# Kernel optimization log

Hardware: AMD Instinct MI355X
Metric: run time of the kernel (lower is better)

## Reference

```python
import jax, jax.numpy as jnp
import numpy as np
import math

INPUT_SIZE = 1024
OUTPUT_SIZE = 1024
QK_SIZE = 1024
B, S = 4, 2048


def setup_inputs() -> dict:
    key = jax.random.key(0)
    ks = jax.random.split(key, 7)
    scale = 1.0 / math.sqrt(INPUT_SIZE)
    return {
        "x": jax.random.normal(ks[0], (B, S, INPUT_SIZE), dtype=jnp.float32),
        "Wq": jax.random.uniform(ks[1], (QK_SIZE, INPUT_SIZE), minval=-scale, maxval=scale, dtype=jnp.float32),
        "bq": jax.random.uniform(ks[2], (QK_SIZE,), minval=-scale, maxval=scale, dtype=jnp.float32),
        "Wk": jax.random.uniform(ks[3], (QK_SIZE, INPUT_SIZE), minval=-scale, maxval=scale, dtype=jnp.float32),
        "bk": jax.random.uniform(ks[4], (QK_SIZE,), minval=-scale, maxval=scale, dtype=jnp.float32),
        "Wv": jax.random.uniform(ks[5], (OUTPUT_SIZE, INPUT_SIZE), minval=-scale, maxval=scale, dtype=jnp.float32),
        "bv": jax.random.uniform(ks[6], (OUTPUT_SIZE,), minval=-scale, maxval=scale, dtype=jnp.float32),
    }


def reference(x, Wq, bq, Wk, bk, Wv, bv):
    # torch Linear: y = x @ W.T + b
    q = jnp.einsum('bsd,ed->bse', x, Wq) + bq  # [B,S,QK]
    k = jnp.einsum('bsd,ed->bse', x, Wk) + bk  # [B,S,QK]
    v = jnp.einsum('bsd,ed->bse', x, Wv) + bv  # [B,S,OUT]
    inv_sqrt_d = 1.0 / math.sqrt(QK_SIZE)
    scores = jnp.einsum('bqe,bke->bqk', q, k) * inv_sqrt_d  # [B,S,S]
    attn = jax.nn.softmax(scores, axis=-1)
    return jnp.einsum('bqk,bko->bqo', attn, v)  # [B,S,OUT]
```

## Files before the change

kernel.cpp:

```cpp
#include <hip/hip_runtime.h>
#include <stdint.h>

typedef unsigned short u16;
typedef __attribute__((ext_vector_type(8))) __bf16 bf16x8;
typedef __attribute__((ext_vector_type(4))) float f32x4;

__device__ __forceinline__ u16 f2bf(float f) {
    union { float f; uint32_t u; } v; v.f = f;
    uint32_t r = (v.u + 0x7FFFu + ((v.u >> 16) & 1u)) >> 16;
    return (u16)r;
}

__device__ __forceinline__ void lds_fence() {
    __asm__ volatile("s_waitcnt lgkmcnt(0)" ::: "memory");
}

#define BARRIER() __builtin_amdgcn_s_barrier()
#define VMW(N)    __asm__ volatile("s_waitcnt vmcnt(" #N ")" ::: "memory")

template<int MODE>
__global__ __launch_bounds__(512, 2) void gemm8(
    const u16* __restrict__ A, const u16* __restrict__ Bt,
    const float* __restrict__ b0, const float* __restrict__ b1, const float* __restrict__ b2,
    u16* __restrict__ o0, u16* __restrict__ o1, u16* __restrict__ o2,
    float* __restrict__ o3, float* __restrict__ lsum,
    int M, int N, int K, long sA, long sB, long sC, float scale)
{
    extern __shared__ __align__(16) u16 smem[];
    constexpr int NIR = (MODE == 3) ? 1 : 2;
    constexpr int NJ  = (MODE == 3) ? 2 : 4;
    constexpr int NHS = (MODE == 3) ? 512 : 1024;

    const int t = threadIdx.x;
    const int lane = t & 63;
    const int wave = t >> 6;
    const int wm = wave >> 2;
    const int wn = wave & 3;

    const int id = blockIdx.x;
    const int xcd = id & 7;
    const int s = id >> 3;
    int bm, bn;
    long bz;
    if (MODE == 0) {
        bm = (xcd * 4 + (s & 3)) * 256;
        bn = (s >> 2) * 256;
        bz = 0;
    } else if (MODE == 2) {
        bz = xcd >> 1;
        bm = ((xcd & 1) * 4 + (s & 3)) * 256;
        bn = (s >> 2) * 256;
    } else {
        bz = xcd >> 1;
        bm = ((xcd & 1) * 4 + (s & 3)) * 256;
        bn = (s >> 2) * 128;
    }

    const u16* Ab = A + bz * sA;
    const u16* Bb = Bt + bz * sB;

    f32x4 acc[8][NJ];
#pragma unroll
    for (int i = 0; i < 8; ++i)
#pragma unroll
        for (int j = 0; j < NJ; ++j)
            acc[i][j] = (f32x4){0.f, 0.f, 0.f, 0.f};

    const int trow = t >> 2;
    const int gcol = ((t & 3) * 8) ^ ((trow & 8) << 1);
    const u16* aRow = Ab + (long)(bm + trow) * K + gcol;
    const u16* bRow = Bb + (long)(bn + trow) * K + gcol;

    auto stage = [&](int buf, int kt, int h, int isB) {
        const u16* g = (isB ? bRow : aRow) + (long)(h * 128) * K + kt * 64;
        u16* d = smem + t * 8 + buf * 32768 + isB * 16384 + h * 8192;
#pragma unroll
        for (int l = 0; l < 2; ++l)
            __builtin_amdgcn_global_load_lds(
                (const __attribute__((address_space(1))) void*)(g + l * 32),
                (__attribute__((address_space(3))) void*)(d + l * 4096), 16, 0, 0);
    };

    const int fm = lane & 15;
    const int fcol = ((lane >> 4) * 8) ^ ((fm & 8) << 1);
    const int aB = wm * 8192 + fm * 32 + fcol;
    const int bB = (MODE == 3)
        ? 16384 + wn * 1024 + fm * 32 + fcol
        : 16384 + (wn >> 1) * 8192 + (wn & 1) * 2048 + fm * 32 + fcol;

    bf16x8 fa[4][2], fb0[NIR][2], fb1[NIR][2];

#define RD_A(BUF, MH) do { \
    _Pragma("unroll") for (int mi = 0; mi < 4; ++mi) \
    _Pragma("unroll") for (int kh = 0; kh < 2; ++kh) \
        fa[mi][kh] = *(const bf16x8*)&smem[(BUF)*32768 + aB + kh*4096 + (MH)*2048 + mi*512]; \
} while (0)

#define RD_B(BUF, NH, DST) do { \
    _Pragma("unroll") for (int ni = 0; ni < NIR; ++ni) \
    _Pragma("unroll") for (int kh = 0; kh < 2; ++kh) \
        DST[ni][kh] = *(const bf16x8*)&smem[(BUF)*32768 + bB + kh*4096 + (NH)*NHS + ni*512]; \
} while (0)

#define QUAD(MH, NH, FB) do { \
    __builtin_amdgcn_s_setprio(1); \
    _Pragma("unroll") for (int mi = 0; mi < 4; ++mi) \
    _Pragma("unroll") for (int ni = 0; ni < NIR; ++ni) \
    _Pragma("unroll") for (int kh = 0; kh < 2; ++kh) \
        acc[(MH)*4+mi][(NH)*NIR+ni] = __builtin_amdgcn_mfma_f32_16x16x32_bf16( \
            fa[mi][kh], FB[ni][kh], acc[(MH)*4+mi][(NH)*NIR+ni], 0, 0, 0); \
    __builtin_amdgcn_s_setprio(0); \
} while (0)

    const int NT = K >> 6;
    const int NI = NT >> 1;

    stage(0, 0, 0, 0); stage(0, 0, 1, 0); stage(0, 0, 0, 1);
    if (MODE != 3) stage(0, 0, 1, 1);
    stage(1, 1, 0, 1); stage(1, 1, 0, 0);
    if (MODE == 3) { VMW(4); } else { VMW(6); }
    BARRIER();

    for (int i = 0; i < NI; ++i) {
        const int knext = 2 * i + 1;
        int ktc = 2 * i + 2; if (ktc >= NT) ktc -= NT;
        const int ktd = ktc + 1;

        RD_A(0, 0); RD_B(0, 0, fb0);
        stage(1, knext, 1, 0);
        BARRIER();
        QUAD(0, 0, fb0);
        if (MODE != 3) VMW(6);
        BARRIER();
        RD_B(0, 1, fb1);
        if (MODE != 3) stage(1, knext, 1, 1);
        BARRIER();
        QUAD(0, 1, fb1);
        BARRIER();
        RD_A(0, 1);
        stage(0, ktc, 0, 1);
        BARRIER();
        QUAD(1, 1, fb1);
        BARRIER();
        stage(0, ktc, 0, 0);
        BARRIER();
        QUAD(1, 0, fb0);
        if (MODE == 3) { VMW(4); } else { VMW(6); }
        BARRIER();
        RD_A(1, 0); RD_B(1, 0, fb0);
        stage(0, ktc, 1, 0);
        BARRIER();
        QUAD(0, 0, fb0);
        if (MODE != 3) VMW(6);
        BARRIER();
        RD_B(1, 1, fb1);
        if (MODE != 3) stage(0, ktc, 1, 1);
        BARRIER();
        QUAD(0, 1, fb1);
        BARRIER();
        RD_A(1, 1);
        stage(1, ktd, 0, 1);
        BARRIER();
        QUAD(1, 1, fb1);
        BARRIER();
        stage(1, ktd, 0, 0);
        BARRIER();
        QUAD(1, 0, fb0);
        if (MODE == 3) { VMW(4); } else { VMW(6); }
        BARRIER();
    }

    VMW(0);
    BARRIER();

    const int cm = (lane >> 4) * 4;
    const int cn = lane & 15;
    u16* Ew = smem + wave * 8192;
    const int gmb = bm + wm * 128;

    if constexpr (MODE == 3) {
        float* Fw = (float*)Ew;
        const int cnb3 = bn + wn * 32;
#pragma unroll
        for (int p = 0; p < 4; ++p) {
            if (p) lds_fence();
#pragma unroll
            for (int m2 = 0; m2 < 2; ++m2) {
                const int mi = p * 2 + m2;
#pragma unroll
                for (int ni = 0; ni < 2; ++ni)
#pragma unroll
                    for (int r = 0; r < 4; ++r)
                        Fw[(m2 * 16 + cm + r) * 36 + ni * 16 + cn] = acc[mi][ni][r];
            }
#pragma unroll
            for (int it = 0; it < 4; ++it) {
                const int row = it * 8 + (lane >> 3);
                const int c4 = (lane & 7) * 4;
                f32x4 w = *(const f32x4*)&Fw[row * 36 + c4];
                const int gm = gmb + p * 32 + row;
                const float inv = __builtin_amdgcn_rcpf(lsum[bz * 2048 + gm]);
                w[0] *= inv; w[1] *= inv; w[2] *= inv; w[3] *= inv;
                *(f32x4*)&o3[bz * sC + (long)gm * N + cnb3 + c4] = w;
            }
        }
    } else if (MODE == 0 && (bn >> 10) == 2) {
        const int ebase = (bn & 1023) + wn * 64;
        float bb[4];
#pragma unroll
        for (int ni = 0; ni < 4; ++ni) bb[ni] = b2[ebase + ni * 16 + cn];
        const long bgi = gmb >> 11;
        const int sbase = gmb & 2047;
#pragma unroll
        for (int p = 0; p < 2; ++p) {
            if (p) lds_fence();
#pragma unroll
            for (int m4 = 0; m4 < 4; ++m4) {
                const int mi = p * 4 + m4;
#pragma unroll
                for (int ni = 0; ni < 4; ++ni) {
                    ushort4 pk;
                    pk.x = f2bf(acc[mi][ni][0] + bb[ni]);
                    pk.y = f2bf(acc[mi][ni][1] + bb[ni]);
                    pk.z = f2bf(acc[mi][ni][2] + bb[ni]);
                    pk.w = f2bf(acc[mi][ni][3] + bb[ni]);
                    *(ushort4*)&Ew[(ni * 16 + cn) * 72 + m4 * 16 + cm] = pk;
                }
            }
#pragma unroll
            for (int it = 0; it < 8; ++it) {
                const int e = it * 8 + (lane >> 3);
                const int s8 = (lane & 7) * 8;
                const uint4 w = *(const uint4*)&Ew[e * 72 + s8];
                *(uint4*)&o2[(((bgi << 10) + ebase + e) << 11) + sbase + p * 64 + s8] = w;
            }
        }
    } else if (MODE == 0) {
        const int sec = bn >> 10;
        u16* C = sec ? o1 : o0;
        const float* bias = sec ? b1 : b0;
        const int ncol0 = (bn & 1023) + wn * 64;
        float bb[4];
#pragma unroll
        for (int ni = 0; ni < 4; ++ni) bb[ni] = bias[ncol0 + ni * 16 + cn];
#pragma unroll
        for (int p = 0; p < 2; ++p) {
            if (p) lds_fence();
#pragma unroll
            for (int m4 = 0; m4 < 4; ++m4) {
                const int mi = p * 4 + m4;
#pragma unroll
                for (int ni = 0; ni < 4; ++ni)
#pragma unroll
                    for (int r = 0; r < 4; ++r)
                        Ew[(m4 * 16 + cm + r) * 72 + ni * 16 + cn] = f2bf(acc[mi][ni][r] + bb[ni]);
            }
#pragma unroll
            for (int it = 0; it < 8; ++it) {
                const int row = it * 8 + (lane >> 3);
                const int c8 = (lane & 7) * 8;
                const uint4 w = *(const uint4*)&Ew[row * 72 + c8];
                *(uint4*)&C[(long)(gmb + p * 64 + row) * 1024 + ncol0 + c8] = w;
            }
        }
    } else {
        const int cnb = bn + wn * 64;
#pragma unroll
        for (int mi = 0; mi < 8; ++mi)
#pragma unroll
            for (int ni = 0; ni < 4; ++ni)
#pragma unroll
                for (int r = 0; r < 4; ++r)
                    acc[mi][ni][r] = __expf(acc[mi][ni][r] * scale);
#pragma unroll
        for (int mi = 0; mi < 8; ++mi) {
#pragma unroll
            for (int r = 0; r < 4; ++r) {
                float sm = acc[mi][0][r] + acc[mi][1][r] + acc[mi][2][r] + acc[mi][3][r];
                sm += __shfl_xor(sm, 1);
                sm += __shfl_xor(sm, 2);
                sm += __shfl_xor(sm, 4);
                sm += __shfl_xor(sm, 8);
                if (cn == 0)
                    atomicAdd(&lsum[bz * 2048 + gmb + mi * 16 + cm + r], sm);
            }
        }
#pragma unroll
        for (int p = 0; p < 2; ++p) {
            if (p) lds_fence();
#pragma unroll
            for (int m4 = 0; m4 < 4; ++m4) {
                const int mi = p * 4 + m4;
#pragma unroll
                for (int ni = 0; ni < 4; ++ni)
#pragma unroll
                    for (int r = 0; r < 4; ++r)
                        Ew[(m4 * 16 + cm + r) * 72 + ni * 16 + cn] = f2bf(acc[mi][ni][r]);
            }
#pragma unroll
            for (int it = 0; it < 8; ++it) {
                const int row = it * 8 + (lane >> 3);
                const int c8 = (lane & 7) * 8;
                const uint4 w = *(const uint4*)&Ew[row * 72 + c8];
                *(uint4*)&o0[bz * sC + (long)(gmb + p * 64 + row) * N + cnb + c8] = w;
            }
        }
    }
}

#undef RD_A
#undef RD_B
#undef QUAD

__global__ __launch_bounds__(256) void cvt_all(
    const float* __restrict__ x, const float* __restrict__ wq,
    const float* __restrict__ wk, const float* __restrict__ wv,
    u16* __restrict__ xb, u16* __restrict__ wb, float* __restrict__ lsum)
{
    const int b = blockIdx.x;
    if (b >= 11264) {
        const long i = (long)(b - 11264) * 1024 + threadIdx.x * 4;
        *(f32x4*)(lsum + i) = (f32x4){0.f, 0.f, 0.f, 0.f};
        return;
    }
    const float* src; u16* dst; long base;
    if (b < 8192)       { src = x;  dst = xb;             base = (long)b * 1024; }
    else if (b < 9216)  { src = wq; dst = wb;             base = (long)(b - 8192) * 1024; }
    else if (b < 10240) { src = wk; dst = wb + (1 << 20); base = (long)(b - 9216) * 1024; }
    else                { src = wv; dst = wb + (2 << 20); base = (long)(b - 10240) * 1024; }
    const long i = base + threadIdx.x * 4;
    const f32x4 f = *(const f32x4*)(src + i);
    ushort4 o;
    o.x = f2bf(f[0]); o.y = f2bf(f[1]); o.z = f2bf(f[2]); o.w = f2bf(f[3]);
    *(ushort4*)(dst + i) = o;
}

extern "C" void kernel_launch(void* const* d_in, const int* in_sizes, int n_in,
                              void* d_out, int out_size, void* d_ws, size_t ws_size,
                              hipStream_t stream) {
    const float* x  = (const float*)d_in[0];
    const float* Wq = (const float*)d_in[1];
    const float* bq = (const float*)d_in[2];
    const float* Wk = (const float*)d_in[3];
    const float* bk = (const float*)d_in[4];
    const float* Wv = (const float*)d_in[5];
    const float* bv = (const float*)d_in[6];
    float* out = (float*)d_out;

    const int B = 4, S = 2048, D = 1024, E = 1024;
    const int M = B * S;
    const size_t LDS = 131072;

    u16* xb  = (u16*)d_ws;
    u16* wb  = xb  + (size_t)M * D;
    u16* qb  = wb  + (size_t)3 * E * D;
    u16* kb  = qb  + (size_t)M * E;
    u16* vbT = kb  + (size_t)M * E;
    u16* sb  = vbT + (size_t)M * E;
    float* lsum = (float*)(sb + (size_t)M * S);

    static bool attr_done = false;
    if (!attr_done) {
        (void)hipFuncSetAttribute((const void*)gemm8<0>, hipFuncAttributeMaxDynamicSharedMemorySize, (int)LDS);
        (void)hipFuncSetAttribute((const void*)gemm8<2>, hipFuncAttributeMaxDynamicSharedMemorySize, (int)LDS);
        (void)hipFuncSetAttribute((const void*)gemm8<3>, hipFuncAttributeMaxDynamicSharedMemorySize, (int)LDS);
        attr_done = true;
    }

    cvt_all<<<11272, 256, 0, stream>>>(x, Wq, Wk, Wv, xb, wb, lsum);

    dim3 blk(512);
    gemm8<0><<<384, blk, LDS, stream>>>(
        xb, wb, bq, bk, bv, qb, kb, vbT, nullptr, nullptr, M, 3 * E, D, 0, 0, 0, 1.f);
    gemm8<2><<<256, blk, LDS, stream>>>(
        qb, kb, nullptr, nullptr, nullptr, sb, nullptr, nullptr, nullptr, lsum,
        S, S, E, (long)S * E, (long)S * E, (long)S * S, 0.03125f);
    gemm8<3><<<256, blk, LDS, stream>>>(
        sb, vbT, nullptr, nullptr, nullptr, nullptr, nullptr, nullptr, out, lsum,
        S, E, S, (long)S * S, (long)E * S, (long)S * E, 1.f);
}
```

Measured before the change: 231.2 us.

## Restructure GEMM main loop into k-half phases with register double-buffered fragments

Reorganizes the GEMM inner loop so each phase computes one M-half over all N columns for a single k-half. The next phase's A/B fragments are loaded into a second register set while the current MFMAs run. Global-to-LDS staging is split into finer per-k-half loads, and the barrier count per iteration drops from 16 to 8. The aim is better overlap of LDS reads and global loads with MFMA work and less barrier overhead, at the cost of more live fragment registers and a more intricate hazard ordering.

```diff
diff --git a/kernel.cpp b/kernel.cpp
--- a/kernel.cpp
+++ b/kernel.cpp
@@ -15,8 +15,8 @@
     __asm__ volatile("s_waitcnt lgkmcnt(0)" ::: "memory");
 }
 
-#define BARRIER() __builtin_amdgcn_s_barrier()
-#define VMW(N)    __asm__ volatile("s_waitcnt vmcnt(" #N ")" ::: "memory")
+#define BAR()  __asm__ volatile("s_barrier" ::: "memory")
+#define VMW(N) __asm__ volatile("s_waitcnt vmcnt(" #N ")" ::: "memory")
 
 template<int MODE>
 __global__ __launch_bounds__(512, 2) void gemm8(
@@ -27,9 +27,7 @@
     int M, int N, int K, long sA, long sB, long sC, float scale)
 {
     extern __shared__ __align__(16) u16 smem[];
-    constexpr int NIR = (MODE == 3) ? 1 : 2;
-    constexpr int NJ  = (MODE == 3) ? 2 : 4;
-    constexpr int NHS = (MODE == 3) ? 512 : 1024;
+    constexpr int NJ = (MODE == 3) ? 2 : 4;
 
     const int t = threadIdx.x;
     const int lane = t & 63;
@@ -71,14 +69,12 @@
     const u16* aRow = Ab + (long)(bm + trow) * K + gcol;
     const u16* bRow = Bb + (long)(bn + trow) * K + gcol;
 
-    auto stage = [&](int buf, int kt, int h, int isB) {
-        const u16* g = (isB ? bRow : aRow) + (long)(h * 128) * K + kt * 64;
-        u16* d = smem + t * 8 + buf * 32768 + isB * 16384 + h * 8192;
-#pragma unroll
-        for (int l = 0; l < 2; ++l)
-            __builtin_amdgcn_global_load_lds(
-                (const __attribute__((address_space(1))) void*)(g + l * 32),
-                (__attribute__((address_space(3))) void*)(d + l * 4096), 16, 0, 0);
+    auto stage1 = [&](int buf, int kt, int isB, int h, int kb) {
+        const u16* g = (isB ? bRow : aRow) + (long)(h * 128) * K + kt * 64 + kb * 32;
+        u16* d = smem + buf * 32768 + isB * 16384 + h * 8192 + kb * 4096 + t * 8;
+        __builtin_amdgcn_global_load_lds(
+            (const __attribute__((address_space(1))) void*)g,
+            (__attribute__((address_space(3))) void*)d, 16, 0, 0);
     };
 
     const int fm = lane & 15;
@@ -88,90 +84,85 @@
         ? 16384 + wn * 1024 + fm * 32 + fcol
         : 16384 + (wn >> 1) * 8192 + (wn & 1) * 2048 + fm * 32 + fcol;
 
-    bf16x8 fa[4][2], fb0[NIR][2], fb1[NIR][2];
-
-#define RD_A(BUF, MH) do { \
+    bf16x8 aCur[4], aNxt[4], bCur[NJ], bNxt[NJ];
+
+#define RD_A(DST, BUF, MH, KH) do { \
     _Pragma("unroll") for (int mi = 0; mi < 4; ++mi) \
-    _Pragma("unroll") for (int kh = 0; kh < 2; ++kh) \
-        fa[mi][kh] = *(const bf16x8*)&smem[(BUF)*32768 + aB + kh*4096 + (MH)*2048 + mi*512]; \
+        DST[mi] = *(const bf16x8*)&smem[(BUF)*32768 + aB + (KH)*4096 + (MH)*2048 + mi*512]; \
 } while (0)
 
-#define RD_B(BUF, NH, DST) do { \
-    _Pragma("unroll") for (int ni = 0; ni < NIR; ++ni) \
-    _Pragma("unroll") for (int kh = 0; kh < 2; ++kh) \
-        DST[ni][kh] = *(const bf16x8*)&smem[(BUF)*32768 + bB + kh*4096 + (NH)*NHS + ni*512]; \
+#define RD_B(DST, BUF, KH) do { \
+    _Pragma("unroll") for (int ni = 0; ni < NJ; ++ni) \
+        DST[ni] = *(const bf16x8*)&smem[(BUF)*32768 + bB + (KH)*4096 + ni*512]; \
 } while (0)
 
-#define QUAD(MH, NH, FB) do { \
+#define PH(MH, FA, FB) do { \
     __builtin_amdgcn_s_setprio(1); \
     _Pragma("unroll") for (int mi = 0; mi < 4; ++mi) \
-    _Pragma("unroll") for (int ni = 0; ni < NIR; ++ni) \
-    _Pragma("unroll") for (int kh = 0; kh < 2; ++kh) \
-        acc[(MH)*4+mi][(NH)*NIR+ni] = __builtin_amdgcn_mfma_f32_16x16x32_bf16( \
-            fa[mi][kh], FB[ni][kh], acc[(MH)*4+mi][(NH)*NIR+ni], 0, 0, 0); \
+    _Pragma("unroll") for (int ni = 0; ni < NJ; ++ni) \
+        acc[(MH)*4+mi][ni] = __builtin_amdgcn_mfma_f32_16x16x32_bf16( \
+            FA[mi], FB[ni], acc[(MH)*4+mi][ni], 0, 0, 0); \
     __builtin_amdgcn_s_setprio(0); \
 } while (0)
 
     const int NT = K >> 6;
     const int NI = NT >> 1;
 
-    stage(0, 0, 0, 0); stage(0, 0, 1, 0); stage(0, 0, 0, 1);
-    if (MODE != 3) stage(0, 0, 1, 1);
-    stage(1, 1, 0, 1); stage(1, 1, 0, 0);
-    if (MODE == 3) { VMW(4); } else { VMW(6); }
-    BARRIER();
+    stage1(0, 0, 1, 0, 0); if (MODE != 3) stage1(0, 0, 1, 1, 0);
+    stage1(0, 0, 0, 0, 0); stage1(0, 0, 0, 1, 0);
+    stage1(0, 0, 1, 0, 1); if (MODE != 3) stage1(0, 0, 1, 1, 1);
+    stage1(0, 0, 0, 0, 1); stage1(0, 0, 0, 1, 1);
+    stage1(1, 1, 1, 0, 0); if (MODE != 3) stage1(1, 1, 1, 1, 0);
+    stage1(1, 1, 0, 0, 0); stage1(1, 1, 0, 1, 0);
+    if (MODE == 3) { VMW(6); } else { VMW(8); }
+    BAR();
+    RD_A(aCur, 0, 0, 0); RD_B(bCur, 0, 0);
 
     for (int i = 0; i < NI; ++i) {
-        const int knext = 2 * i + 1;
-        int ktc = 2 * i + 2; if (ktc >= NT) ktc -= NT;
-        const int ktd = ktc + 1;
-
-        RD_A(0, 0); RD_B(0, 0, fb0);
-        stage(1, knext, 1, 0);
-        BARRIER();
-        QUAD(0, 0, fb0);
-        if (MODE != 3) VMW(6);
-        BARRIER();
-        RD_B(0, 1, fb1);
-        if (MODE != 3) stage(1, knext, 1, 1);
-        BARRIER();
-        QUAD(0, 1, fb1);
-        BARRIER();
-        RD_A(0, 1);
-        stage(0, ktc, 0, 1);
-        BARRIER();
-        QUAD(1, 1, fb1);
-        BARRIER();
-        stage(0, ktc, 0, 0);
-        BARRIER();
-        QUAD(1, 0, fb0);
+        const int t1 = 2 * i + 1;
+        int t2 = 2 * i + 2; if (t2 >= NT) t2 -= NT;
+        int t3 = 2 * i + 3; if (t3 >= NT) t3 -= NT;
+
+        PH(0, aCur, bCur);
+        RD_A(aNxt, 0, 1, 0);
+        stage1(1, t1, 1, 0, 1); if (MODE != 3) stage1(1, t1, 1, 1, 1);
         if (MODE == 3) { VMW(4); } else { VMW(6); }
-        BARRIER();
-        RD_A(1, 0); RD_B(1, 0, fb0);
-        stage(0, ktc, 1, 0);
-        BARRIER();
-        QUAD(0, 0, fb0);
-        if (MODE != 3) VMW(6);
-        BARRIER();
-        RD_B(1, 1, fb1);
-        if (MODE != 3) stage(0, ktc, 1, 1);
-        BARRIER();
-        QUAD(0, 1, fb1);
-        BARRIER();
-        RD_A(1, 1);
-        stage(1, ktd, 0, 1);
-        BARRIER();
-        QUAD(1, 1, fb1);
-        BARRIER();
-        stage(1, ktd, 0, 0);
-        BARRIER();
-        QUAD(1, 0, fb0);
+        BAR();
+        PH(1, aNxt, bCur);
+        RD_A(aCur, 0, 0, 1); RD_B(bNxt, 0, 1);
+        stage1(1, t1, 0, 0, 1); stage1(1, t1, 0, 1, 1);
+        BAR();
+        PH(0, aCur, bNxt);
+        RD_A(aNxt, 0, 1, 1);
+        stage1(0, t2, 1, 0, 0); if (MODE != 3) stage1(0, t2, 1, 1, 0);
         if (MODE == 3) { VMW(4); } else { VMW(6); }
-        BARRIER();
+        BAR();
+        PH(1, aNxt, bNxt);
+        RD_A(aCur, 1, 0, 0); RD_B(bCur, 1, 0);
+        stage1(0, t2, 0, 0, 0); stage1(0, t2, 0, 1, 0);
+        BAR();
+        PH(0, aCur, bCur);
+        RD_A(aNxt, 1, 1, 0);
+        stage1(0, t2, 1, 0, 1); if (MODE != 3) stage1(0, t2, 1, 1, 1);
+        if (MODE == 3) { VMW(4); } else { VMW(6); }
+        BAR();
+        PH(1, aNxt, bCur);
+        RD_A(aCur, 1, 0, 1); RD_B(bNxt, 1, 1);
+        stage1(0, t2, 0, 0, 1); stage1(0, t2, 0, 1, 1);
+        BAR();
+        PH(0, aCur, bNxt);
+        RD_A(aNxt, 1, 1, 1);
+        stage1(1, t3, 1, 0, 0); if (MODE != 3) stage1(1, t3, 1, 1, 0);
+        if (MODE == 3) { VMW(4); } else { VMW(6); }
+        BAR();
+        PH(1, aNxt, bNxt);
+        RD_A(aCur, 0, 0, 0); RD_B(bCur, 0, 0);
+        stage1(1, t3, 0, 0, 0); stage1(1, t3, 0, 1, 0);
+        BAR();
     }
 
     VMW(0);
-    BARRIER();
+    BAR();
 
     const int cm = (lane >> 4) * 4;
     const int cn = lane & 15;
@@ -310,7 +301,7 @@
 
 #undef RD_A
 #undef RD_B
-#undef QUAD
+#undef PH
 
 __global__ __launch_bounds__(256) void cvt_all(
     const float* __restrict__ x, const float* __restrict__ wq,
```

New measurement: 227.9 us. About the same (-1.4%).
